# Performance work log

Measured on AMD Instinct MI355X. Metric: run time of the kernel, lower is better.

## Reference

```python
import math
import jax, jax.numpy as jnp
import numpy as np

D = 512; H = 8; N = 6; DFF = 2048; VS = 32000; VT = 32000
B = 4; S = 1024; T = 1024
EPS = 1e-5


def _pe(length, d):
    pos = jnp.arange(length, dtype=jnp.float32)[:, None]
    div = jnp.exp(jnp.arange(0, d, 2, dtype=jnp.float32) * (-math.log(10000.0) / d))
    pe = jnp.zeros((length, d), jnp.float32)
    pe = pe.at[:, 0::2].set(jnp.sin(pos * div)).at[:, 1::2].set(jnp.cos(pos * div))
    return pe  # [L, D]


def _ln(x, g, b):
    m = x.mean(-1, keepdims=True)
    v = ((x - m) ** 2).mean(-1, keepdims=True)
    return (x - m) / jnp.sqrt(v + EPS) * g + b


def _mha(xq, xkv, w, b, mask):
    # w: [4, D, D], b: [4, D]; mask broadcastable to [B, H, Sq, Sk]
    nb, sq, d = xq.shape
    dk = d // H
    def proj(x, i):
        return (x @ w[i] + b[i]).reshape(x.shape[0], x.shape[1], H, dk).transpose(0, 2, 1, 3)
    q, k, v = proj(xq, 0), proj(xkv, 1), proj(xkv, 2)
    scores = jnp.einsum('bhqd,bhkd->bhqk', q, k) / math.sqrt(dk)
    scores = jnp.where(mask == 0, -1e9, scores)
    p = jax.nn.softmax(scores, axis=-1)
    o = jnp.einsum('bhqk,bhkd->bhqd', p, v).transpose(0, 2, 1, 3).reshape(nb, sq, d)
    return o @ w[3] + b[3]


def _ffn(x, w1, b1, w2, b2):
    return jax.nn.relu(x @ w1 + b1) @ w2 + b2


def _forward(src_emb, tgt_emb,
             enc_attn_w, enc_attn_b, enc_ffn_w1, enc_ffn_b1, enc_ffn_w2, enc_ffn_b2,
             enc_ln_g, enc_ln_b, enc_fg, enc_fb,
             dec_self_w, dec_self_b, dec_src_w, dec_src_b,
             dec_ffn_w1, dec_ffn_b1, dec_ffn_w2, dec_ffn_b2,
             dec_ln_g, dec_ln_b, dec_fg, dec_fb,
             gen_w, gen_b,
             src, tgt, src_mask, tgt_mask):
    # embed + positional encoding (dropout off: eval mode)
    x = src_emb[src] + _pe(src.shape[1], D)[None]
    for i in range(N):
        a = _mha(x, x, enc_attn_w[i], enc_attn_b[i], src_mask)
        x = _ln(x + a, enc_ln_g[i, 0], enc_ln_b[i, 0])
        f = _ffn(x, enc_ffn_w1[i], enc_ffn_b1[i], enc_ffn_w2[i], enc_ffn_b2[i])
        x = _ln(x + f, enc_ln_g[i, 1], enc_ln_b[i, 1])
    memory = _ln(x, enc_fg, enc_fb)

    y = tgt_emb[tgt] + _pe(tgt.shape[1], D)[None]
    for i in range(N):
        a = _mha(y, y, dec_self_w[i], dec_self_b[i], tgt_mask)
        y = _ln(y + a, dec_ln_g[i, 0], dec_ln_b[i, 0])
        a = _mha(y, memory, dec_src_w[i], dec_src_b[i], src_mask)
        y = _ln(y + a, dec_ln_g[i, 1], dec_ln_b[i, 1])
        f = _ffn(y, dec_ffn_w1[i], dec_ffn_b1[i], dec_ffn_w2[i], dec_ffn_b2[i])
        y = _ln(y + f, dec_ln_g[i, 2], dec_ln_b[i, 2])
    y = _ln(y, dec_fg, dec_fb)
    return y @ gen_w + gen_b  # [B, T, VT]


def setup_inputs():
    key = jax.random.key(0)
    ks = iter(jax.random.split(key, 48))
    def w(*shape):
        return jax.random.normal(next(ks), shape, dtype=jnp.float32) * 0.02
    inp = {}
    inp['src_emb'] = w(VS, D)
    inp['tgt_emb'] = w(VT, D)
    inp['enc_attn_w'] = w(N, 4, D, D)
    inp['enc_attn_b'] = jnp.zeros((N, 4, D), jnp.float32)
    inp['enc_ffn_w1'] = w(N, D, DFF)
    inp['enc_ffn_b1'] = jnp.zeros((N, DFF), jnp.float32)
    inp['enc_ffn_w2'] = w(N, DFF, D)
    inp['enc_ffn_b2'] = jnp.zeros((N, D), jnp.float32)
    inp['enc_ln_g'] = jnp.ones((N, 2, D), jnp.float32)
    inp['enc_ln_b'] = jnp.zeros((N, 2, D), jnp.float32)
    inp['enc_fg'] = jnp.ones((D,), jnp.float32)
    inp['enc_fb'] = jnp.zeros((D,), jnp.float32)
    inp['dec_self_w'] = w(N, 4, D, D)
    inp['dec_self_b'] = jnp.zeros((N, 4, D), jnp.float32)
    inp['dec_src_w'] = w(N, 4, D, D)
    inp['dec_src_b'] = jnp.zeros((N, 4, D), jnp.float32)
    inp['dec_ffn_w1'] = w(N, D, DFF)
    inp['dec_ffn_b1'] = jnp.zeros((N, DFF), jnp.float32)
    inp['dec_ffn_w2'] = w(N, DFF, D)
    inp['dec_ffn_b2'] = jnp.zeros((N, D), jnp.float32)
    inp['dec_ln_g'] = jnp.ones((N, 3, D), jnp.float32)
    inp['dec_ln_b'] = jnp.zeros((N, 3, D), jnp.float32)
    inp['dec_fg'] = jnp.ones((D,), jnp.float32)
    inp['dec_fb'] = jnp.zeros((D,), jnp.float32)
    inp['gen_w'] = w(D, VT)
    inp['gen_b'] = jnp.zeros((VT,), jnp.float32)
    inp['src'] = jax.random.randint(next(ks), (B, S), 0, VS)
    inp['tgt'] = jax.random.randint(next(ks), (B, T), 0, VT)
    inp['src_mask'] = jnp.ones((B, 1, 1, S), jnp.int32)
    inp['tgt_mask'] = jnp.tril(jnp.ones((T, T), jnp.int32))[None, None]  # causal [1,1,T,T]
    return inp


def reference(src_emb, tgt_emb, enc_attn_w, enc_attn_b, enc_ffn_w1, enc_ffn_b1,
              enc_ffn_w2, enc_ffn_b2, enc_ln_g, enc_ln_b, enc_fg, enc_fb,
              dec_self_w, dec_self_b, dec_src_w, dec_src_b,
              dec_ffn_w1, dec_ffn_b1, dec_ffn_w2, dec_ffn_b2,
              dec_ln_g, dec_ln_b, dec_fg, dec_fb, gen_w, gen_b,
              src, tgt, src_mask, tgt_mask):
    return _forward(src_emb, tgt_emb, enc_attn_w, enc_attn_b, enc_ffn_w1, enc_ffn_b1,
                    enc_ffn_w2, enc_ffn_b2, enc_ln_g, enc_ln_b, enc_fg, enc_fb,
                    dec_self_w, dec_self_b, dec_src_w, dec_src_b,
                    dec_ffn_w1, dec_ffn_b1, dec_ffn_w2, dec_ffn_b2,
                    dec_ln_g, dec_ln_b, dec_fg, dec_fb, gen_w, gen_b,
                    src, tgt, src_mask, tgt_mask)
```

## Files before the change

kernel.cpp:

```cpp
#include <hip/hip_runtime.h>


typedef __bf16 bf16x8 __attribute__((ext_vector_type(8)));
typedef __bf16 bf16x4 __attribute__((ext_vector_type(4)));
typedef float  f32x4  __attribute__((ext_vector_type(4)));

__device__ __forceinline__ void gload_lds16(const void* g, void* l) {
  __builtin_amdgcn_global_load_lds((__attribute__((address_space(1))) void*)g,
                                   (__attribute__((address_space(3))) void*)l,
                                   16, 0, 0);
}

__device__ __forceinline__ void hard_barrier() {
  asm volatile("" ::: "memory");
  __builtin_amdgcn_sched_barrier(0);
  __builtin_amdgcn_s_barrier();
  __builtin_amdgcn_sched_barrier(0);
  asm volatile("" ::: "memory");
}

template<int EPI>
__global__ __launch_bounds__(256)
void gemm_kernel(const __bf16* __restrict__ A, int lda,
                 const __bf16* __restrict__ BT, int ldb,
                 void* __restrict__ Cv, int ldc,
                 const float* __restrict__ bias, int K,
                 __bf16* __restrict__ qb, __bf16* __restrict__ kb,
                 __bf16* __restrict__ vt, int zoff)
{
  constexpr int BM = 128, BN = 64, BK = 64;
  constexpr int WM = 64, WN = 32, FM = 4, FN = 2;
  constexpr int LA = (BM * BK) / 2048;
  constexpr int LB = (BN * BK) / 2048;
  constexpr int SLOT = (BM + BN) * BK;
  __shared__ __bf16 lds[3 * SLOT];
  const int tid  = threadIdx.x;
  const int lane = tid & 63, wave = tid >> 6;
  const int wr = wave >> 1, wc = wave & 1;
  const int bm = blockIdx.x * BM, bn = blockIdx.y * BN;

  auto stage = [&](int slot, int kt) {
    const char* Ag = (const char*)A;
    const char* Bg = (const char*)BT;
    char* base = (char*)(lds + slot * SLOT);
    const long long k0b = (long long)kt * (BK * 2);
#pragma unroll
    for (int i = 0; i < LA; i++) {
      int t = tid + i * 256;
      int row = t >> 3, cb = (t & 7) << 4;
      int src = cb ^ ((row & 7) << 4);
      gload_lds16(Ag + ((long long)(bm + row) * lda) * 2 + k0b + src, base + t * 16);
    }
#pragma unroll
    for (int i = 0; i < LB; i++) {
      int t = tid + i * 256;
      int row = t >> 3, cb = (t & 7) << 4;
      int src = cb ^ ((row & 7) << 4);
      gload_lds16(Bg + ((long long)(bn + row) * ldb) * 2 + k0b + src,
                  base + BM * BK * 2 + t * 16);
    }
  };

  f32x4 acc[FM][FN] = {};
  const int NT = K / BK;

  stage(0, 0);
  stage(1, 1);

  for (int t = 0; t < NT; t++) {
    if (t < NT - 1) {
      asm volatile("s_waitcnt vmcnt(6)" ::: "memory");
    } else {
      asm volatile("s_waitcnt vmcnt(0)" ::: "memory");
    }
    hard_barrier();
    if (t + 2 < NT) stage((t + 2) % 3, t + 2);
    const char* sA = (const char*)(lds + (t % 3) * SLOT);
    const char* sB = sA + BM * BK * 2;
#pragma unroll
    for (int kk = 0; kk < 2; kk++) {
      const int g = kk * 64 + (lane >> 4) * 16;
      bf16x8 af[FM], bfr[FN];
#pragma unroll
      for (int i = 0; i < FM; i++) {
        int row = wr * WM + i * 16 + (lane & 15);
        af[i] = *(const bf16x8*)(sA + row * 128 + (g ^ ((row & 7) << 4)));
      }
#pragma unroll
      for (int j = 0; j < FN; j++) {
        int row = wc * WN + j * 16 + (lane & 15);
        bfr[j] = *(const bf16x8*)(sB + row * 128 + (g ^ ((row & 7) << 4)));
      }
      __builtin_amdgcn_s_setprio(1);
#pragma unroll
      for (int i = 0; i < FM; i++)
#pragma unroll
        for (int j = 0; j < FN; j++)
          acc[i][j] = __builtin_amdgcn_mfma_f32_16x16x32_bf16(af[i], bfr[j], acc[i][j], 0, 0, 0);
      __builtin_amdgcn_s_setprio(0);
    }
  }

#pragma unroll
  for (int i = 0; i < FM; i++) {
#pragma unroll
    for (int j = 0; j < FN; j++) {
      int row0 = bm + wr * WM + i * 16 + (lane >> 4) * 4;
      int col  = bn + wc * WN + j * 16 + (lane & 15);
      float bv = bias ? bias[col] : 0.f;
      if constexpr (EPI == 2) {
        int z = zoff + (col >> 9);
        int cw = col & 511;
        int b = row0 >> 10, s = row0 & 1023;
        int h = cw >> 6, dk = cw & 63;
        long long bh = b * 8 + h;
        if (z == 2) {
          bf16x4 vv;
#pragma unroll
          for (int r = 0; r < 4; r++) vv[r] = (__bf16)(acc[i][j][r] + bv);
          *(bf16x4*)(vt + (bh << 16) + (dk << 10) + s) = vv;
        } else {
          __bf16* dst = (z == 0) ? qb : kb;
          float sc = (z == 0) ? 0.125f : 1.0f;
#pragma unroll
          for (int r = 0; r < 4; r++)
            dst[(bh << 16) + ((long long)(s + r) << 6) + dk] = (__bf16)((acc[i][j][r] + bv) * sc);
        }
      } else if constexpr (EPI == 1) {
        __bf16* C = (__bf16*)Cv;
#pragma unroll
        for (int r = 0; r < 4; r++)
          C[(long long)(row0 + r) * ldc + col] = (__bf16)fmaxf(acc[i][j][r] + bv, 0.f);
      } else {
        float* C = (float*)Cv;
#pragma unroll
        for (int r = 0; r < 4; r++)
          C[(long long)(row0 + r) * ldc + col] = acc[i][j][r] + bv;
      }
    }
  }
}

template<int CAUSAL>
__global__ __launch_bounds__(256)
void flash_kernel(const __bf16* __restrict__ qb, const __bf16* __restrict__ kb,
                  const __bf16* __restrict__ vt, const int* __restrict__ smask,
                  __bf16* __restrict__ Ob)
{
  __shared__ __bf16 lK[2 * 128 * 64];
  __shared__ __bf16 lV[2 * 64 * 128];
  __shared__ __bf16 lP[4][16 * 128];
  const int bh = blockIdx.y;
  const int b = bh >> 3, h = bh & 7;
  const int q0 = blockIdx.x * 64;
  const int tid = threadIdx.x, lane = tid & 63, w = tid >> 6;
  const char* kh = (const char*)(kb + ((long long)bh << 16));
  const char* vh = (const char*)(vt + ((long long)bh << 16));

  auto stageKV = [&](int buf, int t) {
    int k0 = t * 128;
#pragma unroll
    for (int i = 0; i < 4; i++) {
      int c = tid + i * 256;
      int row = c >> 3, cb = (c & 7) << 4;
      int cl = cb ^ ((row & 7) << 4);
      gload_lds16(kh + (long long)(k0 + row) * 128 + cl, (char*)lK + buf * 16384 + c * 16);
    }
#pragma unroll
    for (int i = 0; i < 4; i++) {
      int c = tid + i * 256;
      int row = c >> 4, cb = (c & 15) << 4;
      int cl = cb ^ ((row & 7) << 4);
      gload_lds16(vh + (long long)row * 2048 + (long long)k0 * 2 + cl, (char*)lV + buf * 16384 + c * 16);
    }
  };

  bf16x8 qa[2];
  {
    const __bf16* qrow = qb + ((long long)bh << 16)
                       + (long long)(q0 + w * 16 + (lane & 15)) * 64 + (lane >> 4) * 8;
    qa[0] = *(const bf16x8*)(qrow);
    qa[1] = *(const bf16x8*)(qrow + 32);
  }
  f32x4 oacc[4] = {};
  float m[4], l[4];
#pragma unroll
  for (int r = 0; r < 4; r++) { m[r] = -3e38f; l[r] = 0.f; }

  const int nt = CAUSAL ? (blockIdx.x / 2 + 1) : 8;
  char* lPw = (char*)lP + w * 4096;
  stageKV(0, 0);

  for (int t = 0; t < nt; t++) {
    const int k0 = t * 128;
    __syncthreads();
    if (t + 1 < nt) stageKV((t + 1) & 1, t + 1);
    char* cK = (char*)lK + (t & 1) * 16384;
    char* cV = (char*)lV + (t & 1) * 16384;

    f32x4 sf[8];
#pragma unroll
    for (int f = 0; f < 8; f++) {
      int row = f * 16 + (lane & 15);
      f32x4 s = {};
#pragma unroll
      for (int ks = 0; ks < 2; ks++) {
        int cb = ks * 64 + (lane >> 4) * 16;
        bf16x8 kf = *(const bf16x8*)(cK + row * 128 + (cb ^ ((row & 7) << 4)));
        s = __builtin_amdgcn_mfma_f32_16x16x32_bf16(qa[ks], kf, s, 0, 0, 0);
      }
      sf[f] = s;
    }

    if (!CAUSAL) {
#pragma unroll
      for (int f = 0; f < 8; f++) {
        if (smask[b * 1024 + k0 + f * 16 + (lane & 15)] == 0) {
#pragma unroll
          for (int r = 0; r < 4; r++) sf[f][r] = -1e30f;
        }
      }
    } else if (t == nt - 1) {
#pragma unroll
      for (int f = 0; f < 8; f++) {
        int kc = k0 + f * 16 + (lane & 15);
#pragma unroll
        for (int r = 0; r < 4; r++) {
          int qr = q0 + w * 16 + (lane >> 4) * 4 + r;
          if (kc > qr) sf[f][r] = -1e30f;
        }
      }
    }

    float mt[4], mn[4], cr[4], rs[4];
#pragma unroll
    for (int r = 0; r < 4; r++) {
      float v = sf[0][r];
#pragma unroll
      for (int f = 1; f < 8; f++) v = fmaxf(v, sf[f][r]);
      mt[r] = v;
    }
#pragma unroll
    for (int o = 1; o < 16; o <<= 1)
#pragma unroll
      for (int r = 0; r < 4; r++) mt[r] = fmaxf(mt[r], __shfl_xor(mt[r], o));
#pragma unroll
    for (int r = 0; r < 4; r++) {
      mn[r] = fmaxf(m[r], mt[r]);
      cr[r] = __expf(m[r] - mn[r]);
      m[r]  = mn[r];
      rs[r] = 0.f;
    }
#pragma unroll
    for (int f = 0; f < 8; f++)
#pragma unroll
      for (int r = 0; r < 4; r++) {
        float p = __expf(sf[f][r] - mn[r]);
        sf[f][r] = p;
        rs[r] += p;
      }
#pragma unroll
    for (int o = 1; o < 16; o <<= 1)
#pragma unroll
      for (int r = 0; r < 4; r++) rs[r] += __shfl_xor(rs[r], o);
#pragma unroll
    for (int r = 0; r < 4; r++) l[r] = l[r] * cr[r] + rs[r];
#pragma unroll
    for (int d = 0; d < 4; d++)
#pragma unroll
      for (int r = 0; r < 4; r++) oacc[d][r] *= cr[r];

#pragma unroll
    for (int f = 0; f < 8; f++) {
      int colB = f * 32 + (lane & 15) * 2;
#pragma unroll
      for (int r = 0; r < 4; r++) {
        int row = (lane >> 4) * 4 + r;
        *(__bf16*)(lPw + row * 256 + (colB ^ ((row & 7) << 4))) = (__bf16)sf[f][r];
      }
    }
    asm volatile("s_waitcnt lgkmcnt(0)" ::: "memory");

#pragma unroll
    for (int ks = 0; ks < 4; ks++) {
      int prow = lane & 15;
      int cb = ks * 64 + (lane >> 4) * 16;
      bf16x8 pa = *(const bf16x8*)(lPw + prow * 256 + (cb ^ ((prow & 7) << 4)));
#pragma unroll
      for (int d = 0; d < 4; d++) {
        int vrow = d * 16 + (lane & 15);
        bf16x8 vf = *(const bf16x8*)(cV + vrow * 256 + (cb ^ ((vrow & 7) << 4)));
        oacc[d] = __builtin_amdgcn_mfma_f32_16x16x32_bf16(pa, vf, oacc[d], 0, 0, 0);
      }
    }
  }

  float inv[4];
#pragma unroll
  for (int r = 0; r < 4; r++) inv[r] = 1.f / l[r];
#pragma unroll
  for (int d = 0; d < 4; d++)
#pragma unroll
    for (int r = 0; r < 4; r++) {
      long long row = b * 1024 + q0 + w * 16 + (lane >> 4) * 4 + r;
      Ob[row * 512 + h * 64 + d * 16 + (lane & 15)] = (__bf16)(oacc[d][r] * inv[r]);
    }
}

__global__ void transpose_w_kernel(const float* __restrict__ W, __bf16* __restrict__ WT,
                                   int K, int N)
{
  __shared__ float t[32][33];
  long long mz = (long long)blockIdx.z * K * N;
  W += mz; WT += mz;
  int n0 = blockIdx.x * 32, k0 = blockIdx.y * 32;
  int tx = threadIdx.x, ty = threadIdx.y;
#pragma unroll
  for (int i = 0; i < 32; i += 8)
    t[ty + i][tx] = W[(long long)(k0 + ty + i) * N + (n0 + tx)];
  __syncthreads();
#pragma unroll
  for (int i = 0; i < 32; i += 8)
    WT[(long long)(n0 + ty + i) * K + (k0 + tx)] = (__bf16)t[tx][ty + i];
}

__global__ void embed_kernel(const float* __restrict__ emb, const int* __restrict__ idx,
                             float* __restrict__ X, __bf16* __restrict__ Xb)
{
  int row = blockIdx.x;
  int s   = row & 1023;
  int tok = idx[row];
  int d0  = threadIdx.x * 4;
  float4 e = *(const float4*)(emb + (long long)tok * 512 + d0);
  const float* ep = (const float*)&e;
  float o[4];
#pragma unroll
  for (int j = 0; j < 4; j++) {
    int d = d0 + j;
    float div = expf((float)(d & ~1) * (-9.210340371976184f / 512.f));
    float ang = (float)s * div;
    float pe  = (d & 1) ? cosf(ang) : sinf(ang);
    o[j] = ep[j] + pe;
  }
  *(float4*)(X + (long long)row * 512 + d0) = *(float4*)o;
  bf16x4 ob;
#pragma unroll
  for (int j = 0; j < 4; j++) ob[j] = (__bf16)o[j];
  *(bf16x4*)(Xb + (long long)row * 512 + d0) = ob;
}

__global__ void ln_kernel(const float* __restrict__ Xin, const float* __restrict__ Rin,
                          const float* __restrict__ g, const float* __restrict__ b,
                          float* __restrict__ Xout, __bf16* __restrict__ Xbout)
{
  int row = blockIdx.x, lane = threadIdx.x;
  long long base = (long long)row * 512 + lane * 8;
  float x[8];
  *(float4*)x       = *(const float4*)(Xin + base);
  *(float4*)(x + 4) = *(const float4*)(Xin + base + 4);
  if (Rin) {
    float4 r0 = *(const float4*)(Rin + base);
    float4 r1 = *(const float4*)(Rin + base + 4);
    x[0] += r0.x; x[1] += r0.y; x[2] += r0.z; x[3] += r0.w;
    x[4] += r1.x; x[5] += r1.y; x[6] += r1.z; x[7] += r1.w;
  }
  float s = 0.f;
#pragma unroll
  for (int i = 0; i < 8; i++) s += x[i];
#pragma unroll
  for (int o = 32; o > 0; o >>= 1) s += __shfl_xor(s, o);
  float mean = s * (1.f / 512.f);
  float v = 0.f;
#pragma unroll
  for (int i = 0; i < 8; i++) { x[i] -= mean; v += x[i] * x[i]; }
#pragma unroll
  for (int o = 32; o > 0; o >>= 1) v += __shfl_xor(v, o);
  float inv = rsqrtf(v * (1.f / 512.f) + 1e-5f);
  int d0 = lane * 8;
  float gg[8], bb[8];
  *(float4*)gg       = *(const float4*)(g + d0);
  *(float4*)(gg + 4) = *(const float4*)(g + d0 + 4);
  *(float4*)bb       = *(const float4*)(b + d0);
  *(float4*)(bb + 4) = *(const float4*)(b + d0 + 4);
  float y[8]; bf16x8 yb;
#pragma unroll
  for (int i = 0; i < 8; i++) {
    y[i] = x[i] * inv * gg[i] + bb[i];
    yb[i] = (__bf16)y[i];
  }
  if (Xout) {
    *(float4*)(Xout + base)     = *(float4*)y;
    *(float4*)(Xout + base + 4) = *(float4*)(y + 4);
  }
  *(bf16x8*)(Xbout + base) = yb;
}

extern "C" void kernel_launch(void* const* d_in, const int* in_sizes, int n_in,
                              void* d_out, int out_size, void* d_ws, size_t ws_size,
                              hipStream_t stream)
{
  (void)in_sizes; (void)n_in; (void)out_size; (void)ws_size;
  const float* src_emb    = (const float*)d_in[0];
  const float* tgt_emb    = (const float*)d_in[1];
  const float* enc_attn_w = (const float*)d_in[2];
  const float* enc_attn_b = (const float*)d_in[3];
  const float* enc_ffn_w1 = (const float*)d_in[4];
  const float* enc_ffn_b1 = (const float*)d_in[5];
  const float* enc_ffn_w2 = (const float*)d_in[6];
  const float* enc_ffn_b2 = (const float*)d_in[7];
  const float* enc_ln_g   = (const float*)d_in[8];
  const float* enc_ln_b   = (const float*)d_in[9];
  const float* enc_fg     = (const float*)d_in[10];
  const float* enc_fb     = (const float*)d_in[11];
  const float* dec_self_w = (const float*)d_in[12];
  const float* dec_self_b = (const float*)d_in[13];
  const float* dec_src_w  = (const float*)d_in[14];
  const float* dec_src_b  = (const float*)d_in[15];
  const float* dec_ffn_w1 = (const float*)d_in[16];
  const float* dec_ffn_b1 = (const float*)d_in[17];
  const float* dec_ffn_w2 = (const float*)d_in[18];
  const float* dec_ffn_b2 = (const float*)d_in[19];
  const float* dec_ln_g   = (const float*)d_in[20];
  const float* dec_ln_b   = (const float*)d_in[21];
  const float* dec_fg     = (const float*)d_in[22];
  const float* dec_fb     = (const float*)d_in[23];
  const float* gen_w      = (const float*)d_in[24];
  const float* gen_b      = (const float*)d_in[25];
  const int*   src        = (const int*)d_in[26];
  const int*   tgt        = (const int*)d_in[27];
  const int*   src_mask   = (const int*)d_in[28];

  float* out = (float*)d_out;

  char* wp = (char*)d_ws;
  auto alloc = [&](size_t bytes) { void* p = (void*)wp; wp += (bytes + 255) & ~(size_t)255; return p; };
  __bf16* TWea = (__bf16*)alloc(24ull * 262144 * 2);
  __bf16* TWe1 = (__bf16*)alloc(6ull * 1048576 * 2);
  __bf16* TWe2 = (__bf16*)alloc(6ull * 1048576 * 2);
  __bf16* TWds = (__bf16*)alloc(24ull * 262144 * 2);
  __bf16* TWdx = (__bf16*)alloc(24ull * 262144 * 2);
  __bf16* TWd1 = (__bf16*)alloc(6ull * 1048576 * 2);
  __bf16* TWd2 = (__bf16*)alloc(6ull * 1048576 * 2);
  float*  X    = (float*) alloc(4096ull * 512 * 4);
  __bf16* Xb   = (__bf16*)alloc(4096ull * 512 * 2);
  __bf16* MEMb = (__bf16*)alloc(4096ull * 512 * 2);
  float*  R    = (float*) alloc(4096ull * 512 * 4);
  __bf16* qb   = (__bf16*)alloc(32ull * 1024 * 64 * 2);
  __bf16* kb   = (__bf16*)alloc(32ull * 1024 * 64 * 2);
  __bf16* vt   = (__bf16*)alloc(32ull * 1024 * 64 * 2);
  __bf16* Ob   = (__bf16*)alloc(4096ull * 512 * 2);
  __bf16* Fb   = qb;
  __bf16* GENT = TWea;

  transpose_w_kernel<<<dim3(16, 16, 24), dim3(32, 8), 0, stream>>>(enc_attn_w, TWea, 512, 512);
  transpose_w_kernel<<<dim3(64, 16, 6),  dim3(32, 8), 0, stream>>>(enc_ffn_w1, TWe1, 512, 2048);
  transpose_w_kernel<<<dim3(16, 64, 6),  dim3(32, 8), 0, stream>>>(enc_ffn_w2, TWe2, 2048, 512);
  transpose_w_kernel<<<dim3(16, 16, 24), dim3(32, 8), 0, stream>>>(dec_self_w, TWds, 512, 512);
  transpose_w_kernel<<<dim3(16, 16, 24), dim3(32, 8), 0, stream>>>(dec_src_w,  TWdx, 512, 512);
  transpose_w_kernel<<<dim3(64, 16, 6),  dim3(32, 8), 0, stream>>>(dec_ffn_w1, TWd1, 512, 2048);
  transpose_w_kernel<<<dim3(16, 64, 6),  dim3(32, 8), 0, stream>>>(dec_ffn_w2, TWd2, 2048, 512);

  auto attention = [&](const __bf16* wt, const float* bptr, int causal,
                       const __bf16* Aq, const __bf16* Akv) {
    if (Aq == Akv) {
      gemm_kernel<2><<<dim3(32, 24), 256, 0, stream>>>(
          Aq, 512, wt, 512, nullptr, 0, bptr, 512, qb, kb, vt, 0);
    } else {
      gemm_kernel<2><<<dim3(32, 8), 256, 0, stream>>>(
          Aq, 512, wt, 512, nullptr, 0, bptr, 512, qb, kb, vt, 0);
      gemm_kernel<2><<<dim3(32, 16), 256, 0, stream>>>(
          Akv, 512, wt + 262144, 512, nullptr, 0, bptr + 512, 512, qb, kb, vt, 1);
    }
    if (causal)
      flash_kernel<1><<<dim3(16, 32), 256, 0, stream>>>(qb, kb, vt, nullptr, Ob);
    else
      flash_kernel<0><<<dim3(16, 32), 256, 0, stream>>>(qb, kb, vt, src_mask, Ob);
    gemm_kernel<0><<<dim3(32, 8), 256, 0, stream>>>(
        Ob, 512, wt + 3 * 262144, 512, R, 512, bptr + 3 * 512, 512,
        nullptr, nullptr, nullptr, 0);
  };

  auto ffn = [&](const __bf16* w1t, const float* b1, const __bf16* w2t, const float* b2) {
    gemm_kernel<1><<<dim3(32, 32), 256, 0, stream>>>(
        Xb, 512, w1t, 512, Fb, 2048, b1, 512, nullptr, nullptr, nullptr, 0);
    gemm_kernel<0><<<dim3(32, 8), 256, 0, stream>>>(
        Fb, 2048, w2t, 2048, R, 512, b2, 2048, nullptr, nullptr, nullptr, 0);
  };

  embed_kernel<<<4096, 128, 0, stream>>>(src_emb, src, X, Xb);
  for (int i = 0; i < 6; i++) {
    attention(TWea + (long long)i * 1048576, enc_attn_b + i * 2048, 0, Xb, Xb);
    ln_kernel<<<4096, 64, 0, stream>>>(X, R, enc_ln_g + i * 1024, enc_ln_b + i * 1024, X, Xb);
    ffn(TWe1 + (long long)i * 1048576, enc_ffn_b1 + i * 2048,
        TWe2 + (long long)i * 1048576, enc_ffn_b2 + i * 512);
    ln_kernel<<<4096, 64, 0, stream>>>(X, R, enc_ln_g + i * 1024 + 512, enc_ln_b + i * 1024 + 512, X, Xb);
  }
  ln_kernel<<<4096, 64, 0, stream>>>(X, nullptr, enc_fg, enc_fb, nullptr, MEMb);

  transpose_w_kernel<<<dim3(1000, 16, 1), dim3(32, 8), 0, stream>>>(gen_w, GENT, 512, 32000);

  embed_kernel<<<4096, 128, 0, stream>>>(tgt_emb, tgt, X, Xb);
  for (int i = 0; i < 6; i++) {
    attention(TWds + (long long)i * 1048576, dec_self_b + i * 2048, 1, Xb, Xb);
    ln_kernel<<<4096, 64, 0, stream>>>(X, R, dec_ln_g + i * 1536, dec_ln_b + i * 1536, X, Xb);

    attention(TWdx + (long long)i * 1048576, dec_src_b + i * 2048, 0, Xb, MEMb);
    ln_kernel<<<4096, 64, 0, stream>>>(X, R, dec_ln_g + i * 1536 + 512, dec_ln_b + i * 1536 + 512, X, Xb);

    ffn(TWd1 + (long long)i * 1048576, dec_ffn_b1 + i * 2048,
        TWd2 + (long long)i * 1048576, dec_ffn_b2 + i * 512);
    ln_kernel<<<4096, 64, 0, stream>>>(X, R, dec_ln_g + i * 1536 + 1024, dec_ln_b + i * 1536 + 1024, X, Xb);
  }
  ln_kernel<<<4096, 64, 0, stream>>>(X, nullptr, dec_fg, dec_fb, nullptr, Xb);

  gemm_kernel<0><<<dim3(32, 500), 256, 0, stream>>>(
      Xb, 512, GENT, 512, out, 32000, gen_b, 512, nullptr, nullptr, nullptr, 0);
}
```

Before: 2.076 ms.

## Add dedicated generator GEMM with triple-buffered LDS, XCD swizzle and staged stores

Replaces the generic GEMM used for the final vocabulary projection with a specialized kernel. It uses 128x64 tiles, a three-slot LDS pipeline fed by direct global-to-LDS loads, and a block index remap that spreads tiles across the 8 XCDs. The epilogue stages fp32 results through LDS so output writes become coalesced 16-byte stores. The aim is to cut memory-bound cost on the large 4096x32000 fp32 output, at the cost of more LDS use and a hardcoded grid.

Result: no change. 2.110 ms (+1.6%).

```diff
diff --git a/kernel.cpp b/kernel.cpp
--- a/kernel.cpp
+++ b/kernel.cpp
@@ -138,6 +138,112 @@
           C[(long long)(row0 + r) * ldc + col] = acc[i][j][r] + bv;
       }
     }
+  }
+}
+
+__global__ __launch_bounds__(256)
+void gemm_gen_kernel(const __bf16* __restrict__ A, int lda,
+                     const __bf16* __restrict__ BT, int ldb,
+                     float* __restrict__ C, int ldc,
+                     const float* __restrict__ bias, int K, int nbx)
+{
+  constexpr int BM = 128, BN = 64, BK = 64;
+  constexpr int WM = 64, WN = 32, FM = 4, FN = 2;
+  constexpr int LA = (BM * BK) / 2048;
+  constexpr int LB = (BN * BK) / 2048;
+  constexpr int SLOT = (BM + BN) * BK;
+  __shared__ __bf16 lds[3 * SLOT];
+  const int tid  = threadIdx.x;
+  const int lane = tid & 63, wave = tid >> 6;
+  const int wr = wave >> 1, wc = wave & 1;
+  const int cpx = gridDim.x >> 3;
+  const int wg  = (blockIdx.x & 7) * cpx + (blockIdx.x >> 3);
+  const int bm  = (wg % nbx) * BM;
+  const int bn  = (wg / nbx) * BN;
+
+  auto stage = [&](int slot, int kt) {
+    const char* Ag = (const char*)A;
+    const char* Bg = (const char*)BT;
+    char* base = (char*)(lds + slot * SLOT);
+    const long long k0b = (long long)kt * (BK * 2);
+#pragma unroll
+    for (int i = 0; i < LA; i++) {
+      int t = tid + i * 256;
+      int row = t >> 3, cb = (t & 7) << 4;
+      int src = cb ^ ((row & 7) << 4);
+      gload_lds16(Ag + ((long long)(bm + row) * lda) * 2 + k0b + src, base + t * 16);
+    }
+#pragma unroll
+    for (int i = 0; i < LB; i++) {
+      int t = tid + i * 256;
+      int row = t >> 3, cb = (t & 7) << 4;
+      int src = cb ^ ((row & 7) << 4);
+      gload_lds16(Bg + ((long long)(bn + row) * ldb) * 2 + k0b + src,
+                  base + BM * BK * 2 + t * 16);
+    }
+  };
+
+  f32x4 acc[FM][FN] = {};
+  const int NT = K / BK;
+
+  stage(0, 0);
+  stage(1, 1);
+
+  for (int t = 0; t < NT; t++) {
+    if (t < NT - 1) {
+      asm volatile("s_waitcnt vmcnt(6)" ::: "memory");
+    } else {
+      asm volatile("s_waitcnt vmcnt(0)" ::: "memory");
+    }
+    hard_barrier();
+    if (t + 2 < NT) stage((t + 2) % 3, t + 2);
+    const char* sA = (const char*)(lds + (t % 3) * SLOT);
+    const char* sB = sA + BM * BK * 2;
+#pragma unroll
+    for (int kk = 0; kk < 2; kk++) {
+      const int g = kk * 64 + (lane >> 4) * 16;
+      bf16x8 af[FM], bfr[FN];
+#pragma unroll
+      for (int i = 0; i < FM; i++) {
+        int row = wr * WM + i * 16 + (lane & 15);
+        af[i] = *(const bf16x8*)(sA + row * 128 + (g ^ ((row & 7) << 4)));
+      }
+#pragma unroll
+      for (int j = 0; j < FN; j++) {
+        int row = wc * WN + j * 16 + (lane & 15);
+        bfr[j] = *(const bf16x8*)(sB + row * 128 + (g ^ ((row & 7) << 4)));
+      }
+      __builtin_amdgcn_s_setprio(1);
+#pragma unroll
+      for (int i = 0; i < FM; i++)
+#pragma unroll
+        for (int j = 0; j < FN; j++)
+          acc[i][j] = __builtin_amdgcn_mfma_f32_16x16x32_bf16(af[i], bfr[j], acc[i][j], 0, 0, 0);
+      __builtin_amdgcn_s_setprio(0);
+    }
+  }
+
+  __syncthreads();
+  float* ct = (float*)lds;
+#pragma unroll
+  for (int i = 0; i < FM; i++) {
+#pragma unroll
+    for (int j = 0; j < FN; j++) {
+      int lrow = wr * WM + i * 16 + (lane >> 4) * 4;
+      int lcol = wc * WN + j * 16 + (lane & 15);
+      float bv = bias[bn + lcol];
+#pragma unroll
+      for (int r = 0; r < 4; r++)
+        ct[(lrow + r) * 68 + lcol] = acc[i][j][r] + bv;
+    }
+  }
+  __syncthreads();
+#pragma unroll
+  for (int it = 0; it < 8; it++) {
+    int idx = tid + it * 256;
+    int row = idx >> 4, c4 = (idx & 15) * 4;
+    f32x4 v = *(const f32x4*)(ct + row * 68 + c4);
+    *(f32x4*)(C + (long long)(bm + row) * ldc + bn + c4) = v;
   }
 }
 
@@ -513,6 +619,6 @@
   }
   ln_kernel<<<4096, 64, 0, stream>>>(X, nullptr, dec_fg, dec_fb, nullptr, Xb);
 
-  gemm_kernel<0><<<dim3(32, 500), 256, 0, stream>>>(
-      Xb, 512, GENT, 512, out, 32000, gen_b, 512, nullptr, nullptr, nullptr, 0);
-}
+  gemm_gen_kernel<<<16000, 256, 0, stream>>>(
+      Xb, 512, GENT, 512, out, 32000, gen_b, 512, 32);
+}
```
